# Kernel tuning notes

Measured on AMD Instinct MI355X. Metric: run time of the kernel, lower is better.

## Reference

```python
import jax, jax.numpy as jnp
import numpy as np

B, S, D = 2, 2048, 1024
H, HD = 16, 64
G, E, M = 2, 8, 1024
EPS = 1e-5


def setup_inputs() -> dict:
    key = jax.random.key(0)
    ks = jax.random.split(key, 20)
    s = 0.02
    return {
        "input": jax.random.normal(ks[0], (B, S, D), jnp.float32),
        "Wq": s * jax.random.normal(ks[1], (D, H * HD), jnp.float32),
        "bq": jnp.zeros((H * HD,), jnp.float32),
        "Wk": s * jax.random.normal(ks[2], (D, H * HD), jnp.float32),
        "bk": jnp.zeros((H * HD,), jnp.float32),
        "Wv": s * jax.random.normal(ks[3], (D, H * HD), jnp.float32),
        "bv": jnp.zeros((H * HD,), jnp.float32),
        "Wo": s * jax.random.normal(ks[4], (H * HD, D), jnp.float32),
        "bo": jnp.zeros((D,), jnp.float32),
        "ln1_g": jnp.ones((D,), jnp.float32),
        "ln1_b": jnp.zeros((D,), jnp.float32),
        "gate_W": s * jax.random.normal(ks[5], (G, D, E), jnp.float32),
        "gate_b": jnp.zeros((G, E), jnp.float32),
        "eW1": s * jax.random.normal(ks[6], (G, E, D, M), jnp.float32),
        "eb1": jnp.zeros((G, E, M), jnp.float32),
        "eW2": s * jax.random.normal(ks[7], (G, E, M, D), jnp.float32),
        "eb2": jnp.zeros((G, E, D), jnp.float32),
        "ln2_g": jnp.ones((D,), jnp.float32),
        "ln2_b": jnp.zeros((D,), jnp.float32),
    }


def _layer_norm(x, g, b):
    mu = jnp.mean(x, axis=-1, keepdims=True)
    var = jnp.mean(jnp.square(x - mu), axis=-1, keepdims=True)
    return (x - mu) * jax.lax.rsqrt(var + EPS) * g + b


def _attention(x, Wq, bq, Wk, bk, Wv, bv, Wo, bo):
    q = (x @ Wq + bq).reshape(B, S, H, HD)
    k = (x @ Wk + bk).reshape(B, S, H, HD)
    v = (x @ Wv + bv).reshape(B, S, H, HD)
    scores = jnp.einsum("bqhd,bkhd->bhqk", q, k) * (1.0 / np.sqrt(HD))
    causal = jnp.tril(jnp.ones((S, S), bool))  # block_size tril mask
    scores = jnp.where(causal, scores, jnp.float32(-1e9))
    probs = jax.nn.softmax(scores, axis=-1)
    out = jnp.einsum("bhqk,bkhd->bqhd", probs, v).reshape(B, S, H * HD)
    return out @ Wo + bo


def _moe(h, gate_W, gate_b, eW1, eb1, eW2, eb2):
    # per-gate softmax over that gate's experts
    gates = jax.nn.softmax(jnp.einsum("bsd,gde->bsge", h, gate_W) + gate_b, axis=-1)
    hid = jax.nn.relu(jnp.einsum("bsd,gedm->bsgem", h, eW1) + eb1)
    exp_out = jnp.einsum("bsgem,gemd->bsged", hid, eW2) + eb2
    # gate-weighted combine, averaged over the n_gates gates
    return jnp.einsum("bsge,bsged->bsd", gates, exp_out) / G


def reference(input, Wq, bq, Wk, bk, Wv, bv, Wo, bo, ln1_g, ln1_b,
              gate_W, gate_b, eW1, eb1, eW2, eb2, ln2_g, ln2_b):
    attn = _attention(input, Wq, bq, Wk, bk, Wv, bv, Wo, bo)
    normed = _layer_norm(attn + input, ln1_g, ln1_b)
    moe_out = _moe(normed, gate_W, gate_b, eW1, eb1, eW2, eb2)
    return _layer_norm(moe_out + normed, ln2_g, ln2_b)
```

## Files before the change

kernel.cpp:

```cpp
#include <hip/hip_runtime.h>

#define BB 2
#define SS 2048
#define DD 1024
#define HH 16
#define HDD 64
#define TT 4096
#define GG 2
#define EE 8
#define MM 1024
#define NEXP 16

typedef __bf16 bf16;
typedef __attribute__((ext_vector_type(8))) __bf16 bf16x8;
typedef __attribute__((ext_vector_type(4))) float f32x4;

__device__ __forceinline__ void async_ld16(void* lds, const void* g) {
  __builtin_amdgcn_global_load_lds((const __attribute__((address_space(1))) unsigned int*)g,
                                   (__attribute__((address_space(3))) unsigned int*)lds,
                                   16, 0, 0);
}

static const long OFF_WQKVT = 0;
static const long OFF_WOT   = OFF_WQKVT + 6291456L;
static const long OFF_W1T   = OFF_WOT   + 2097152L;
static const long OFF_W2T   = OFF_W1T   + 33554432L;
static const long OFF_XBF   = OFF_W2T   + 33554432L;
static const long OFF_REGA  = OFF_XBF   + 8388608L;
static const long OFF_H1F   = OFF_REGA  + 33554432L;
static const long OFF_H1B   = OFF_H1F   + 16777216L;
static const long OFF_GATES = OFF_H1B   + 8388608L;
static const long OFF_BQKV  = OFF_GATES + 262144L;
static const long OFF_MOE   = OFF_BQKV  + 12288L;
static const long WS_NEED   = OFF_MOE   + 16777216L;

__global__ void cast_f32_bf16(const float* __restrict__ in, bf16* __restrict__ out, long n) {
  long idx = ((long)blockIdx.x * blockDim.x + threadIdx.x) * 4;
  if (idx + 3 < n) {
    float4 v = *(const float4*)(in + idx);
    out[idx]   = (bf16)v.x; out[idx+1] = (bf16)v.y;
    out[idx+2] = (bf16)v.z; out[idx+3] = (bf16)v.w;
  }
}

__global__ void transpose_cast(const float* __restrict__ in, bf16* __restrict__ out,
                               int R, int C, long in_zstride, long out_zoff, long out_ld) {
  __shared__ float tile[32][33];
  int z = blockIdx.z;
  const float* src = in + (long)z * in_zstride;
  bf16* dst = out + (long)z * out_zoff;
  int c0 = blockIdx.x * 32, r0 = blockIdx.y * 32;
  int tx = threadIdx.x, ty = threadIdx.y;
  for (int i = 0; i < 4; i++) {
    int r = ty + i * 8;
    tile[r][tx] = src[(long)(r0 + r) * C + c0 + tx];
  }
  __syncthreads();
  for (int i = 0; i < 4; i++) {
    int n = ty + i * 8;
    dst[(long)(c0 + n) * out_ld + r0 + tx] = (bf16)tile[tx][n];
  }
}

__global__ void transpose_cast4(const float* __restrict__ s0, const float* __restrict__ s1,
                                const float* __restrict__ s2, const float* __restrict__ s3,
                                bf16* __restrict__ d0, bf16* __restrict__ d1,
                                bf16* __restrict__ d2, bf16* __restrict__ d3) {
  __shared__ float tile[32][33];
  int z = blockIdx.z;
  const float* src = (z == 0) ? s0 : (z == 1) ? s1 : (z == 2) ? s2 : s3;
  bf16* dst = (z == 0) ? d0 : (z == 1) ? d1 : (z == 2) ? d2 : d3;
  int c0 = blockIdx.x * 32, r0 = blockIdx.y * 32;
  int tx = threadIdx.x, ty = threadIdx.y;
  for (int i = 0; i < 4; i++) {
    int r = ty + i * 8;
    tile[r][tx] = src[(long)(r0 + r) * 1024 + c0 + tx];
  }
  __syncthreads();
  for (int i = 0; i < 4; i++) {
    int n = ty + i * 8;
    dst[(long)(c0 + n) * 1024 + r0 + tx] = (bf16)tile[tx][n];
  }
}

__global__ void pack3(const float* __restrict__ a, const float* __restrict__ b,
                      const float* __restrict__ c, float* __restrict__ out, int n) {
  int i = blockIdx.x * blockDim.x + threadIdx.x;
  if (i < n) out[i] = a[i];
  else if (i < 2 * n) out[i] = b[i - n];
  else if (i < 3 * n) out[i] = c[i - 2 * n];
}

template<int EPI>
__global__ __launch_bounds__(256, 3)
void gemm_bt(const bf16* __restrict__ A, const bf16* __restrict__ BT,
             int M, int N, int K, int lda, int ldb,
             const float* __restrict__ bias, int bias_off,
             const float* __restrict__ resid,
             const float* __restrict__ gates, int gate_base,
             float* __restrict__ outf, bf16* __restrict__ outb, int ldo,
             float* __restrict__ p1a, float* __restrict__ p1b) {
  __shared__ bf16 As[128 * 64];
  __shared__ bf16 Bs[128 * 64];
  int gx = gridDim.x, gy = gridDim.y;
  int l = blockIdx.x + gx * blockIdx.y;
  int xcd = l & 7, idx = l >> 3;
  int RG = gx >> 2, CG = gy >> 1;
  int bmB = (xcd >> 1) * RG + (idx % RG);
  int bnB = (xcd & 1) * CG + (idx / RG);
  int bm = bmB * 128;
  int bn = bnB * 128;
  long koff = (long)blockIdx.z * K;
  A += koff; BT += koff;
  int tid = threadIdx.x;
  int wave = tid >> 6, lane = tid & 63;
  int quad = lane >> 4, l16 = lane & 15;
  int wr = wave >> 1, wc = wave & 1;

  f32x4 acc[4][4];
  for (int i = 0; i < 4; i++)
    for (int j = 0; j < 4; j++) acc[i][j] = (f32x4){0.f, 0.f, 0.f, 0.f};

  for (int k0 = 0; k0 < K; k0 += 64) {
    __syncthreads();
    for (int i = 0; i < 4; i++) {
      int s = (i * 4 + wave) * 64 + lane;
      int r = s >> 3, cp = s & 7, c = cp ^ (r & 7);
      async_ld16((char*)As + s * 16, A + (long)(bm + r) * lda + k0 + c * 8);
      async_ld16((char*)Bs + s * 16, BT + (long)(bn + r) * ldb + k0 + c * 8);
    }
    __syncthreads();
    for (int kk = 0; kk < 64; kk += 32) {
      int cc = quad + (kk >> 3);
      bf16x8 af[4], bfr[4];
      for (int i = 0; i < 4; i++) {
        int row = wr * 64 + i * 16 + l16;
        af[i] = *(const bf16x8*)((char*)As + row * 128 + (cc ^ (row & 7)) * 16);
      }
      for (int j = 0; j < 4; j++) {
        int row = wc * 64 + j * 16 + l16;
        bfr[j] = *(const bf16x8*)((char*)Bs + row * 128 + (cc ^ (row & 7)) * 16);
      }
      for (int i = 0; i < 4; i++)
        for (int j = 0; j < 4; j++)
          acc[i][j] = __builtin_amdgcn_mfma_f32_16x16x32_bf16(af[i], bfr[j], acc[i][j], 0, 0, 0);
    }
  }

  float* dst = outf;
  if (EPI == 3 && blockIdx.z == 1)
    dst = (bm < 2048) ? p1a : (p1b - 2048L * 1024);

  for (int i = 0; i < 4; i++)
    for (int j = 0; j < 4; j++) {
      int colg = bn + wc * 64 + j * 16 + l16;
      for (int r = 0; r < 4; r++) {
        int rowg = bm + wr * 64 + i * 16 + quad * 4 + r;
        float v = acc[i][j][r];
        if (EPI == 0) {
          v += bias[colg];
          outb[(long)rowg * ldo + colg] = (bf16)v;
        } else if (EPI == 1) {
          v += bias[colg] + resid[(long)rowg * ldo + colg];
          outf[(long)rowg * ldo + colg] = v;
        } else if (EPI == 2) {
          v += bias[bias_off + colg];
          v = v > 0.f ? v : 0.f;
          float gsc = gates[(long)rowg * NEXP + gate_base + (colg >> 10)] * 0.5f;
          outb[(long)rowg * ldo + colg] = (bf16)(v * gsc);
        } else {
          dst[(long)rowg * ldo + colg] += v;
        }
      }
    }
}

#define VPAD 132
__global__ __launch_bounds__(256, 3)
void flash_attn(const bf16* __restrict__ qkv, bf16* __restrict__ attn) {
  int qbp = blockIdx.y & 15;
  int bh = blockIdx.x + 8 * (blockIdx.y >> 4);
  int b = bh >> 4, h = bh & 15;
  int tid = threadIdx.x;
  int wave = tid >> 6, lane = tid & 63, quad = lane >> 4, l16 = lane & 15;

  __shared__ bf16 Ks[128 * 64];
  __shared__ bf16 Vt[64][VPAD];
  __shared__ bf16 VsPs[4 * 16 * VPAD];
  bf16* Vs = VsPs;
  bf16* PsB = VsPs;

  const long rs = 3072;
  const bf16* Qp = qkv + (long)b * SS * rs + (long)h * HDD;
  const bf16* Kp = Qp + 1024;
  const bf16* Vp = Qp + 2048;

  for (int half = 0; half < 2; half++) {
    int qb = half ? qbp : (31 - qbp);
    bf16x8 qf[2];
    {
      int qrow = qb * 64 + wave * 16 + l16;
      for (int c = 0; c < 2; c++)
        qf[c] = *(const bf16x8*)(Qp + (long)qrow * rs + c * 32 + quad * 8);
    }
    f32x4 o[4];
    for (int j = 0; j < 4; j++) o[j] = (f32x4){0.f, 0.f, 0.f, 0.f};
    float lrow[4] = {0.f, 0.f, 0.f, 0.f};

    int niter = (qb >> 1) + 1;
    for (int kt = 0; kt < niter; kt++) {
      __syncthreads();
      for (int i = 0; i < 4; i++) {
        int s = (i * 4 + wave) * 64 + lane;
        int r = s >> 3, cp = s & 7, c = cp ^ (r & 7);
        async_ld16((char*)Ks + s * 16, Kp + (long)(kt * 128 + r) * rs + c * 8);
        async_ld16((char*)Vs + s * 16, Vp + (long)(kt * 128 + r) * rs + c * 8);
      }
      __syncthreads();

      {
        int d = lane, kb = wave * 32;
        bf16 tmp[32];
        for (int k2 = 0; k2 < 32; k2++) {
          int k = kb + k2;
          tmp[k2] = *((const bf16*)((char*)Vs + k * 128 + (((d >> 3) ^ (k & 7)) * 16) + (d & 7) * 2));
        }
        for (int j = 0; j < 4; j++)
          *(bf16x8*)(&Vt[d][kb + j * 8]) = *(bf16x8*)(&tmp[j * 8]);
      }

      f32x4 s8[8];
      for (int n = 0; n < 8; n++) s8[n] = (f32x4){0.f, 0.f, 0.f, 0.f};
      for (int c = 0; c < 2; c++) {
        int cc = quad + c * 4;
        for (int n = 0; n < 8; n++) {
          int row = n * 16 + l16;
          bf16x8 kf = *(const bf16x8*)((char*)Ks + row * 128 + (cc ^ (row & 7)) * 16);
          s8[n] = __builtin_amdgcn_mfma_f32_16x16x32_bf16(qf[c], kf, s8[n], 0, 0, 0);
        }
      }

      const float sc = 0.125f;
      const float M0 = 12.0f;
      float psum[4] = {0.f, 0.f, 0.f, 0.f};
      if (kt == niter - 1) {
        for (int n = 0; n < 8; n++) {
          int key = kt * 128 + n * 16 + l16;
          for (int r = 0; r < 4; r++) {
            int q = qb * 64 + wave * 16 + quad * 4 + r;
            float e = (key <= q) ? __expf(s8[n][r] * sc - M0) : 0.f;
            s8[n][r] = e; psum[r] += e;
          }
        }
      } else {
        for (int n = 0; n < 8; n++)
          for (int r = 0; r < 4; r++) {
            float e = __expf(s8[n][r] * sc - M0);
            s8[n][r] = e; psum[r] += e;
          }
      }
      for (int r = 0; r < 4; r++) {
        for (int d2 = 1; d2 < 16; d2 <<= 1) psum[r] += __shfl_xor(psum[r], d2, 64);
        lrow[r] += psum[r];
      }

      __syncthreads();

      for (int n = 0; n < 8; n++)
        for (int r = 0; r < 4; r++)
          PsB[(wave * 16 + quad * 4 + r) * VPAD + n * 16 + l16] = (bf16)s8[n][r];
      for (int c = 0; c < 4; c++) {
        bf16x8 pf = *(const bf16x8*)(&PsB[(wave * 16 + l16) * VPAD + c * 32 + quad * 8]);
        for (int j = 0; j < 4; j++) {
          bf16x8 vf = *(const bf16x8*)(&Vt[j * 16 + l16][c * 32 + quad * 8]);
          o[j] = __builtin_amdgcn_mfma_f32_16x16x32_bf16(pf, vf, o[j], 0, 0, 0);
        }
      }
    }

    for (int j = 0; j < 4; j++)
      for (int r = 0; r < 4; r++) {
        int t = b * SS + qb * 64 + wave * 16 + quad * 4 + r;
        int col = h * 64 + j * 16 + l16;
        attn[(long)t * 1024 + col] = (bf16)(o[j][r] / lrow[r]);
      }
  }
}

__global__ __launch_bounds__(256)
void layernorm(const float* __restrict__ in, const float* __restrict__ resid,
               const float* __restrict__ p1a, const float* __restrict__ p1b,
               const float* __restrict__ g, const float* __restrict__ b,
               float* __restrict__ outf, bf16* __restrict__ outb) {
  int row = blockIdx.x;
  int tid = threadIdx.x;
  const float* x = in + (long)row * DD;
  const float* ex = nullptr;
  if (p1a) ex = (row < 2048) ? (p1a + (long)row * DD) : (p1b + (long)(row - 2048) * DD);
  float v[4];
  for (int i = 0; i < 4; i++) {
    int c = tid + i * 256;
    v[i] = x[c];
    if (resid) v[i] += resid[(long)row * DD + c];
    if (ex) v[i] += ex[c];
  }
  __shared__ float red[8];
  float s = v[0] + v[1] + v[2] + v[3];
  for (int d = 1; d < 64; d <<= 1) s += __shfl_xor(s, d, 64);
  if ((tid & 63) == 0) red[tid >> 6] = s;
  __syncthreads();
  float mean = (red[0] + red[1] + red[2] + red[3]) * (1.0f / DD);
  float s2 = 0.f;
  for (int i = 0; i < 4; i++) { float d = v[i] - mean; s2 += d * d; }
  for (int d = 1; d < 64; d <<= 1) s2 += __shfl_xor(s2, d, 64);
  if ((tid & 63) == 0) red[4 + (tid >> 6)] = s2;
  __syncthreads();
  float var = (red[4] + red[5] + red[6] + red[7]) * (1.0f / DD);
  float rstd = rsqrtf(var + 1e-5f);
  for (int i = 0; i < 4; i++) {
    int c = tid + i * 256;
    float y = (v[i] - mean) * rstd * g[c] + b[c];
    if (outf) outf[(long)row * DD + c] = y;
    if (outb) outb[(long)row * DD + c] = (bf16)y;
  }
}

__global__ __launch_bounds__(256)
void gate_moe_init(const float* __restrict__ h, const float* __restrict__ gW,
                   const float* __restrict__ gb, const float* __restrict__ eb2,
                   float* __restrict__ gates, float* __restrict__ moe,
                   float* __restrict__ p1a, float* __restrict__ p1b) {
  int wave = threadIdx.x >> 6, lane = threadIdx.x & 63;
  int t = blockIdx.x * 4 + wave;
  float acc[16];
  for (int i = 0; i < 16; i++) acc[i] = 0.f;
  for (int kk = 0; kk < 16; kk++) {
    int k = lane + kk * 64;
    float xv = h[(long)t * DD + k];
    for (int g2 = 0; g2 < 2; g2++)
      for (int e = 0; e < 8; e++)
        acc[g2 * 8 + e] += xv * gW[(long)g2 * DD * EE + (long)k * EE + e];
  }
  for (int i = 0; i < 16; i++)
    for (int d = 1; d < 64; d <<= 1) acc[i] += __shfl_xor(acc[i], d, 64);
  __shared__ float gsh[4][16];
  if (lane == 0) {
    float out[16];
    for (int g2 = 0; g2 < 2; g2++) {
      float mx = -1e30f;
      for (int e = 0; e < 8; e++) { acc[g2 * 8 + e] += gb[g2 * 8 + e]; mx = fmaxf(mx, acc[g2 * 8 + e]); }
      float sum = 0.f;
      for (int e = 0; e < 8; e++) { out[g2 * 8 + e] = __expf(acc[g2 * 8 + e] - mx); sum += out[g2 * 8 + e]; }
      for (int e = 0; e < 8; e++) out[g2 * 8 + e] /= sum;
    }
    for (int i = 0; i < 16; i++) { gsh[wave][i] = out[i]; gates[(long)t * 16 + i] = out[i]; }
  }
  __syncthreads();
  float gr[16];
  for (int i = 0; i < 16; i++) gr[i] = gsh[wave][i];
  float* mrow = moe + (long)t * DD;
  float* prow = (t < 2048) ? (p1a + (long)t * DD) : (p1b + (long)(t - 2048) * DD);
  for (int i = 0; i < 16; i++) {
    int d = lane + i * 64;
    float s = 0.f;
    for (int ge = 0; ge < 16; ge++) s += gr[ge] * eb2[ge * 1024 + d];
    mrow[d] = s * 0.5f;
    prow[d] = 0.f;
  }
}

extern "C" void kernel_launch(void* const* d_in, const int* in_sizes, int n_in,
                              void* d_out, int out_size, void* d_ws, size_t ws_size,
                              hipStream_t stream) {
  const float* X     = (const float*)d_in[0];
  const float* Wq    = (const float*)d_in[1];
  const float* bq    = (const float*)d_in[2];
  const float* Wk    = (const float*)d_in[3];
  const float* bk    = (const float*)d_in[4];
  const float* Wv    = (const float*)d_in[5];
  const float* bv    = (const float*)d_in[6];
  const float* Wo    = (const float*)d_in[7];
  const float* bo    = (const float*)d_in[8];
  const float* ln1g  = (const float*)d_in[9];
  const float* ln1b  = (const float*)d_in[10];
  const float* gateW = (const float*)d_in[11];
  const float* gateb = (const float*)d_in[12];
  const float* eW1   = (const float*)d_in[13];
  const float* eb1   = (const float*)d_in[14];
  const float* eW2   = (const float*)d_in[15];
  const float* eb2   = (const float*)d_in[16];
  const float* ln2g  = (const float*)d_in[17];
  const float* ln2b  = (const float*)d_in[18];

  if (ws_size < (size_t)WS_NEED) return;

  char* ws = (char*)d_ws;
  bf16* WqkvT  = (bf16*)(ws + OFF_WQKVT);
  bf16* WoT    = (bf16*)(ws + OFF_WOT);
  bf16* W1T    = (bf16*)(ws + OFF_W1T);
  bf16* W2T    = (bf16*)(ws + OFF_W2T);
  bf16* Xbf    = (bf16*)(ws + OFF_XBF);
  bf16* qkvb   = (bf16*)(ws + OFF_REGA);
  bf16* attnb  = (bf16*)(ws + OFF_REGA + 25165824L);
  bf16* hid    = (bf16*)(ws + OFF_REGA);
  float* h1f   = (float*)(ws + OFF_H1F);
  bf16* h1b    = (bf16*)(ws + OFF_H1B);
  float* gates = (float*)(ws + OFF_GATES);
  float* bqkv  = (float*)(ws + OFF_BQKV);
  float* moe   = (float*)(ws + OFF_MOE);
  float* p1a   = (float*)(ws + OFF_WQKVT);
  float* p1b   = (float*)(ws + OFF_XBF);

  dim3 tcb(32, 8);
  transpose_cast4<<<dim3(32, 32, 4), tcb, 0, stream>>>(Wq, Wk, Wv, Wo,
                                                       WqkvT, WqkvT + 1024L * 1024,
                                                       WqkvT + 2048L * 1024, WoT);
  transpose_cast<<<dim3(32, 32, 16), tcb, 0, stream>>>(eW1, W1T, 1024, 1024, 1048576L, 1048576L, 1024);
  transpose_cast<<<dim3(32, 32, 16), tcb, 0, stream>>>(eW2, W2T, 1024, 1024, 1048576L, 1024L, 16384);
  cast_f32_bf16<<<4096, 256, 0, stream>>>(X, Xbf, 4194304L);
  pack3<<<12, 256, 0, stream>>>(bq, bk, bv, bqkv, 1024);

  gemm_bt<0><<<dim3(32, 24, 1), 256, 0, stream>>>(Xbf, WqkvT, TT, 3072, 1024, 1024, 1024,
                                                  bqkv, 0, nullptr, nullptr, 0, nullptr, qkvb, 3072, nullptr, nullptr);
  flash_attn<<<dim3(8, 64), 256, 0, stream>>>(qkvb, attnb);
  gemm_bt<1><<<dim3(32, 8, 1), 256, 0, stream>>>(attnb, WoT, TT, 1024, 1024, 1024, 1024,
                                                 bo, 0, X, nullptr, 0, moe, nullptr, 1024, nullptr, nullptr);
  layernorm<<<4096, 256, 0, stream>>>(moe, nullptr, nullptr, nullptr, ln1g, ln1b, h1f, h1b);
  gate_moe_init<<<1024, 256, 0, stream>>>(h1f, gateW, gateb, eb2, gates, moe, p1a, p1b);
  for (int c = 0; c < 4; c++) {
    gemm_bt<2><<<dim3(32, 32, 1), 256, 0, stream>>>(h1b, W1T + (long)c * 4096 * 1024, TT, 4096, 1024, 1024, 1024,
                                                    eb1, c * 4096, nullptr, gates, c * 4, nullptr, hid, 4096, nullptr, nullptr);
    gemm_bt<3><<<dim3(32, 8, 2), 256, 0, stream>>>(hid, W2T + (long)c * 4096, TT, 1024, 2048, 4096, 16384,
                                                   nullptr, 0, nullptr, nullptr, 0, moe, nullptr, 1024, p1a, p1b);
  }
  layernorm<<<4096, 256, 0, stream>>>(moe, h1f, p1a, p1b, ln2g, ln2b, (float*)d_out, nullptr);
}
```

Baseline: 778.8 us.

## Pre-transpose V globally, split-K Wo GEMM, fold expert bias into final layernorm

A new vtrans kernel writes V transposed to global memory, so flash attention can async-load V^T tiles straight into LDS. This removes the per-tile in-LDS V transpose and one barrier, and P is now staged through a per-wave transposed buffer. The Wo projection becomes a split-K GEMM whose second partial is summed inside layernorm1. The eb2 gate-weighted bias and the moe/partial zero-init move out of the gate kernel: the first W2 chunk stores instead of accumulating, and the bias is added in the final layernorm. The two expert transpose launches are merged into one. This adds an extra kernel and global traffic for V^T, and LDS reads for the P fragment are now scalar gathers.

New measurement: 807.2 us. 1.04x slower.

```diff
diff --git a/kernel.cpp b/kernel.cpp
--- a/kernel.cpp
+++ b/kernel.cpp
@@ -13,6 +13,7 @@
 
 typedef __bf16 bf16;
 typedef __attribute__((ext_vector_type(8))) __bf16 bf16x8;
+typedef __attribute__((ext_vector_type(4))) __bf16 bf16x4;
 typedef __attribute__((ext_vector_type(4))) float f32x4;
 
 __device__ __forceinline__ void async_ld16(void* lds, const void* g) {
@@ -43,25 +44,6 @@
   }
 }
 
-__global__ void transpose_cast(const float* __restrict__ in, bf16* __restrict__ out,
-                               int R, int C, long in_zstride, long out_zoff, long out_ld) {
-  __shared__ float tile[32][33];
-  int z = blockIdx.z;
-  const float* src = in + (long)z * in_zstride;
-  bf16* dst = out + (long)z * out_zoff;
-  int c0 = blockIdx.x * 32, r0 = blockIdx.y * 32;
-  int tx = threadIdx.x, ty = threadIdx.y;
-  for (int i = 0; i < 4; i++) {
-    int r = ty + i * 8;
-    tile[r][tx] = src[(long)(r0 + r) * C + c0 + tx];
-  }
-  __syncthreads();
-  for (int i = 0; i < 4; i++) {
-    int n = ty + i * 8;
-    dst[(long)(c0 + n) * out_ld + r0 + tx] = (bf16)tile[tx][n];
-  }
-}
-
 __global__ void transpose_cast4(const float* __restrict__ s0, const float* __restrict__ s1,
                                 const float* __restrict__ s2, const float* __restrict__ s3,
                                 bf16* __restrict__ d0, bf16* __restrict__ d1,
@@ -83,12 +65,51 @@
   }
 }
 
+__global__ void transpose_experts(const float* __restrict__ eW1, const float* __restrict__ eW2,
+                                  bf16* __restrict__ W1T, bf16* __restrict__ W2T) {
+  __shared__ float tile[32][33];
+  int z = blockIdx.z;
+  const float* src; bf16* dstp; long ld;
+  if (z < 16) { src = eW1 + (long)z * 1048576; dstp = W1T + (long)z * 1048576; ld = 1024; }
+  else        { src = eW2 + (long)(z - 16) * 1048576; dstp = W2T + (long)(z - 16) * 1024; ld = 16384; }
+  int c0 = blockIdx.x * 32, r0 = blockIdx.y * 32;
+  int tx = threadIdx.x, ty = threadIdx.y;
+  for (int i = 0; i < 4; i++) {
+    int r = ty + i * 8;
+    tile[r][tx] = src[(long)(r0 + r) * 1024 + c0 + tx];
+  }
+  __syncthreads();
+  for (int i = 0; i < 4; i++) {
+    int n = ty + i * 8;
+    dstp[(long)(c0 + n) * ld + r0 + tx] = (bf16)tile[tx][n];
+  }
+}
+
 __global__ void pack3(const float* __restrict__ a, const float* __restrict__ b,
                       const float* __restrict__ c, float* __restrict__ out, int n) {
   int i = blockIdx.x * blockDim.x + threadIdx.x;
   if (i < n) out[i] = a[i];
   else if (i < 2 * n) out[i] = b[i - n];
   else if (i < 3 * n) out[i] = c[i - 2 * n];
+}
+
+__global__ void vtrans(const bf16* __restrict__ qkv, bf16* __restrict__ vtg) {
+  __shared__ bf16 T[128][72];
+  int bh = blockIdx.x, s0 = blockIdx.y * 128;
+  int b = bh >> 4, h = bh & 15;
+  const bf16* Vp = qkv + (long)b * SS * 3072 + 2048 + h * 64;
+  int tid = threadIdx.x;
+  for (int i = 0; i < 4; i++) {
+    int idx = tid + i * 256; int r = idx >> 3, c = idx & 7;
+    *(bf16x8*)&T[r][c * 8] = *(const bf16x8*)(Vp + (long)(s0 + r) * 3072 + c * 8);
+  }
+  __syncthreads();
+  for (int i = 0; i < 4; i++) {
+    int idx = tid + i * 256; int d = idx >> 4, sc = idx & 15;
+    bf16 tmp[8];
+    for (int j = 0; j < 8; j++) tmp[j] = T[sc * 8 + j][d];
+    *(bf16x8*)(vtg + ((long)bh * 64 + d) * 2048 + s0 + sc * 8) = *(bf16x8*)tmp;
+  }
 }
 
 template<int EPI>
@@ -106,10 +127,8 @@
   int l = blockIdx.x + gx * blockIdx.y;
   int xcd = l & 7, idx = l >> 3;
   int RG = gx >> 2, CG = gy >> 1;
-  int bmB = (xcd >> 1) * RG + (idx % RG);
-  int bnB = (xcd & 1) * CG + (idx / RG);
-  int bm = bmB * 128;
-  int bn = bnB * 128;
+  int bm = ((xcd >> 1) * RG + (idx % RG)) * 128;
+  int bn = ((xcd & 1) * CG + (idx / RG)) * 128;
   long koff = (long)blockIdx.z * K;
   A += koff; BT += koff;
   int tid = threadIdx.x;
@@ -148,7 +167,7 @@
   }
 
   float* dst = outf;
-  if (EPI == 3 && blockIdx.z == 1)
+  if ((EPI == 3 || EPI == 4) && blockIdx.z == 1)
     dst = (bm < 2048) ? p1a : (p1b - 2048L * 1024);
 
   for (int i = 0; i < 4; i++)
@@ -161,23 +180,29 @@
           v += bias[colg];
           outb[(long)rowg * ldo + colg] = (bf16)v;
         } else if (EPI == 1) {
-          v += bias[colg] + resid[(long)rowg * ldo + colg];
-          outf[(long)rowg * ldo + colg] = v;
+          if (blockIdx.z == 0) {
+            v += bias[colg] + resid[(long)rowg * ldo + colg];
+            outf[(long)rowg * ldo + colg] = v;
+          } else {
+            p1a[(long)rowg * ldo + colg] = v;
+          }
         } else if (EPI == 2) {
           v += bias[bias_off + colg];
           v = v > 0.f ? v : 0.f;
           float gsc = gates[(long)rowg * NEXP + gate_base + (colg >> 10)] * 0.5f;
           outb[(long)rowg * ldo + colg] = (bf16)(v * gsc);
+        } else if (EPI == 3) {
+          dst[(long)rowg * ldo + colg] += v;
         } else {
-          dst[(long)rowg * ldo + colg] += v;
+          dst[(long)rowg * ldo + colg] = v;
         }
       }
     }
 }
 
-#define VPAD 132
 __global__ __launch_bounds__(256, 3)
-void flash_attn(const bf16* __restrict__ qkv, bf16* __restrict__ attn) {
+void flash_attn(const bf16* __restrict__ qkv, const bf16* __restrict__ vtg,
+                bf16* __restrict__ attn) {
   int qbp = blockIdx.y & 15;
   int bh = blockIdx.x + 8 * (blockIdx.y >> 4);
   int b = bh >> 4, h = bh & 15;
@@ -185,15 +210,13 @@
   int wave = tid >> 6, lane = tid & 63, quad = lane >> 4, l16 = lane & 15;
 
   __shared__ bf16 Ks[128 * 64];
-  __shared__ bf16 Vt[64][VPAD];
-  __shared__ bf16 VsPs[4 * 16 * VPAD];
-  bf16* Vs = VsPs;
-  bf16* PsB = VsPs;
+  __shared__ bf16 VtL[64 * 128];
+  __shared__ bf16 PsT[4][128][20];
 
   const long rs = 3072;
   const bf16* Qp = qkv + (long)b * SS * rs + (long)h * HDD;
   const bf16* Kp = Qp + 1024;
-  const bf16* Vp = Qp + 2048;
+  const bf16* Vg = vtg + (long)bh * 64 * 2048;
 
   for (int half = 0; half < 2; half++) {
     int qb = half ? qbp : (31 - qbp);
@@ -214,20 +237,13 @@
         int s = (i * 4 + wave) * 64 + lane;
         int r = s >> 3, cp = s & 7, c = cp ^ (r & 7);
         async_ld16((char*)Ks + s * 16, Kp + (long)(kt * 128 + r) * rs + c * 8);
-        async_ld16((char*)Vs + s * 16, Vp + (long)(kt * 128 + r) * rs + c * 8);
+      }
+      for (int i = 0; i < 4; i++) {
+        int s = (i * 4 + wave) * 64 + lane;
+        int r = s >> 4, cp = s & 15, gc = (cp & 8) | ((cp ^ r) & 7);
+        async_ld16((char*)VtL + s * 16, Vg + (long)r * 2048 + kt * 128 + gc * 8);
       }
       __syncthreads();
-
-      {
-        int d = lane, kb = wave * 32;
-        bf16 tmp[32];
-        for (int k2 = 0; k2 < 32; k2++) {
-          int k = kb + k2;
-          tmp[k2] = *((const bf16*)((char*)Vs + k * 128 + (((d >> 3) ^ (k & 7)) * 16) + (d & 7) * 2));
-        }
-        for (int j = 0; j < 4; j++)
-          *(bf16x8*)(&Vt[d][kb + j * 8]) = *(bf16x8*)(&tmp[j * 8]);
-      }
 
       f32x4 s8[8];
       for (int n = 0; n < 8; n++) s8[n] = (f32x4){0.f, 0.f, 0.f, 0.f};
@@ -264,16 +280,20 @@
         lrow[r] += psum[r];
       }
 
-      __syncthreads();
-
-      for (int n = 0; n < 8; n++)
-        for (int r = 0; r < 4; r++)
-          PsB[(wave * 16 + quad * 4 + r) * VPAD + n * 16 + l16] = (bf16)s8[n][r];
+      for (int n = 0; n < 8; n++) {
+        bf16x4 p4;
+        for (int r = 0; r < 4; r++) p4[r] = (bf16)s8[n][r];
+        *(bf16x4*)(&PsT[wave][n * 16 + l16][quad * 4]) = p4;
+      }
       for (int c = 0; c < 4; c++) {
-        bf16x8 pf = *(const bf16x8*)(&PsB[(wave * 16 + l16) * VPAD + c * 32 + quad * 8]);
-        for (int j = 0; j < 4; j++) {
-          bf16x8 vf = *(const bf16x8*)(&Vt[j * 16 + l16][c * 32 + quad * 8]);
-          o[j] = __builtin_amdgcn_mfma_f32_16x16x32_bf16(pf, vf, o[j], 0, 0, 0);
+        bf16x8 pf;
+        for (int j = 0; j < 8; j++)
+          pf[j] = PsT[wave][c * 32 + quad * 8 + j][l16];
+        for (int j2 = 0; j2 < 4; j2++) {
+          int d = j2 * 16 + l16;
+          int k4 = c * 4 + quad;
+          bf16x8 vf = *(const bf16x8*)((char*)VtL + d * 256 + (((k4 & 8) | ((k4 ^ d) & 7)) * 16));
+          o[j2] = __builtin_amdgcn_mfma_f32_16x16x32_bf16(pf, vf, o[j2], 0, 0, 0);
         }
       }
     }
@@ -287,9 +307,11 @@
   }
 }
 
+template<bool GB>
 __global__ __launch_bounds__(256)
 void layernorm(const float* __restrict__ in, const float* __restrict__ resid,
                const float* __restrict__ p1a, const float* __restrict__ p1b,
+               const float* __restrict__ gates, const float* __restrict__ eb2,
                const float* __restrict__ g, const float* __restrict__ b,
                float* __restrict__ outf, bf16* __restrict__ outb) {
   int row = blockIdx.x;
@@ -297,12 +319,22 @@
   const float* x = in + (long)row * DD;
   const float* ex = nullptr;
   if (p1a) ex = (row < 2048) ? (p1a + (long)row * DD) : (p1b + (long)(row - 2048) * DD);
+  __shared__ float gsh[16];
+  if (GB) {
+    if (tid < 16) gsh[tid] = gates[(long)row * 16 + tid] * 0.5f;
+    __syncthreads();
+  }
   float v[4];
   for (int i = 0; i < 4; i++) {
     int c = tid + i * 256;
     v[i] = x[c];
     if (resid) v[i] += resid[(long)row * DD + c];
     if (ex) v[i] += ex[c];
+    if (GB) {
+      float s = 0.f;
+      for (int ge = 0; ge < 16; ge++) s += gsh[ge] * eb2[ge * 1024 + c];
+      v[i] += s;
+    }
   }
   __shared__ float red[8];
   float s = v[0] + v[1] + v[2] + v[3];
@@ -326,10 +358,8 @@
 }
 
 __global__ __launch_bounds__(256)
-void gate_moe_init(const float* __restrict__ h, const float* __restrict__ gW,
-                   const float* __restrict__ gb, const float* __restrict__ eb2,
-                   float* __restrict__ gates, float* __restrict__ moe,
-                   float* __restrict__ p1a, float* __restrict__ p1b) {
+void gate_kernel(const float* __restrict__ h, const float* __restrict__ gW,
+                 const float* __restrict__ gb, float* __restrict__ gates) {
   int wave = threadIdx.x >> 6, lane = threadIdx.x & 63;
   int t = blockIdx.x * 4 + wave;
   float acc[16];
@@ -343,7 +373,6 @@
   }
   for (int i = 0; i < 16; i++)
     for (int d = 1; d < 64; d <<= 1) acc[i] += __shfl_xor(acc[i], d, 64);
-  __shared__ float gsh[4][16];
   if (lane == 0) {
     float out[16];
     for (int g2 = 0; g2 < 2; g2++) {
@@ -353,19 +382,7 @@
       for (int e = 0; e < 8; e++) { out[g2 * 8 + e] = __expf(acc[g2 * 8 + e] - mx); sum += out[g2 * 8 + e]; }
       for (int e = 0; e < 8; e++) out[g2 * 8 + e] /= sum;
     }
-    for (int i = 0; i < 16; i++) { gsh[wave][i] = out[i]; gates[(long)t * 16 + i] = out[i]; }
-  }
-  __syncthreads();
-  float gr[16];
-  for (int i = 0; i < 16; i++) gr[i] = gsh[wave][i];
-  float* mrow = moe + (long)t * DD;
-  float* prow = (t < 2048) ? (p1a + (long)t * DD) : (p1b + (long)(t - 2048) * DD);
-  for (int i = 0; i < 16; i++) {
-    int d = lane + i * 64;
-    float s = 0.f;
-    for (int ge = 0; ge < 16; ge++) s += gr[ge] * eb2[ge * 1024 + d];
-    mrow[d] = s * 0.5f;
-    prow[d] = 0.f;
+    for (int i = 0; i < 16; i++) gates[(long)t * 16 + i] = out[i];
   }
 }
 
@@ -403,11 +420,13 @@
   bf16* qkvb   = (bf16*)(ws + OFF_REGA);
   bf16* attnb  = (bf16*)(ws + OFF_REGA + 25165824L);
   bf16* hid    = (bf16*)(ws + OFF_REGA);
+  float* pWo   = (float*)(ws + OFF_REGA);
   float* h1f   = (float*)(ws + OFF_H1F);
   bf16* h1b    = (bf16*)(ws + OFF_H1B);
   float* gates = (float*)(ws + OFF_GATES);
   float* bqkv  = (float*)(ws + OFF_BQKV);
   float* moe   = (float*)(ws + OFF_MOE);
+  bf16* VtG    = (bf16*)(ws + OFF_MOE);
   float* p1a   = (float*)(ws + OFF_WQKVT);
   float* p1b   = (float*)(ws + OFF_XBF);
 
@@ -415,23 +434,29 @@
   transpose_cast4<<<dim3(32, 32, 4), tcb, 0, stream>>>(Wq, Wk, Wv, Wo,
                                                        WqkvT, WqkvT + 1024L * 1024,
                                                        WqkvT + 2048L * 1024, WoT);
-  transpose_cast<<<dim3(32, 32, 16), tcb, 0, stream>>>(eW1, W1T, 1024, 1024, 1048576L, 1048576L, 1024);
-  transpose_cast<<<dim3(32, 32, 16), tcb, 0, stream>>>(eW2, W2T, 1024, 1024, 1048576L, 1024L, 16384);
+  transpose_experts<<<dim3(32, 32, 32), tcb, 0, stream>>>(eW1, eW2, W1T, W2T);
   cast_f32_bf16<<<4096, 256, 0, stream>>>(X, Xbf, 4194304L);
   pack3<<<12, 256, 0, stream>>>(bq, bk, bv, bqkv, 1024);
 
   gemm_bt<0><<<dim3(32, 24, 1), 256, 0, stream>>>(Xbf, WqkvT, TT, 3072, 1024, 1024, 1024,
                                                   bqkv, 0, nullptr, nullptr, 0, nullptr, qkvb, 3072, nullptr, nullptr);
-  flash_attn<<<dim3(8, 64), 256, 0, stream>>>(qkvb, attnb);
-  gemm_bt<1><<<dim3(32, 8, 1), 256, 0, stream>>>(attnb, WoT, TT, 1024, 1024, 1024, 1024,
-                                                 bo, 0, X, nullptr, 0, moe, nullptr, 1024, nullptr, nullptr);
-  layernorm<<<4096, 256, 0, stream>>>(moe, nullptr, nullptr, nullptr, ln1g, ln1b, h1f, h1b);
-  gate_moe_init<<<1024, 256, 0, stream>>>(h1f, gateW, gateb, eb2, gates, moe, p1a, p1b);
+  vtrans<<<dim3(32, 16), 256, 0, stream>>>(qkvb, VtG);
+  flash_attn<<<dim3(8, 64), 256, 0, stream>>>(qkvb, VtG, attnb);
+  gemm_bt<1><<<dim3(32, 8, 2), 256, 0, stream>>>(attnb, WoT, TT, 1024, 512, 1024, 1024,
+                                                 bo, 0, X, nullptr, 0, moe, nullptr, 1024, pWo, nullptr);
+  layernorm<false><<<4096, 256, 0, stream>>>(moe, nullptr, pWo, pWo + 2048L * 1024,
+                                             nullptr, nullptr, ln1g, ln1b, h1f, h1b);
+  gate_kernel<<<1024, 256, 0, stream>>>(h1f, gateW, gateb, gates);
   for (int c = 0; c < 4; c++) {
     gemm_bt<2><<<dim3(32, 32, 1), 256, 0, stream>>>(h1b, W1T + (long)c * 4096 * 1024, TT, 4096, 1024, 1024, 1024,
                                                     eb1, c * 4096, nullptr, gates, c * 4, nullptr, hid, 4096, nullptr, nullptr);
-    gemm_bt<3><<<dim3(32, 8, 2), 256, 0, stream>>>(hid, W2T + (long)c * 4096, TT, 1024, 2048, 4096, 16384,
-                                                   nullptr, 0, nullptr, nullptr, 0, moe, nullptr, 1024, p1a, p1b);
-  }
-  layernorm<<<4096, 256, 0, stream>>>(moe, h1f, p1a, p1b, ln2g, ln2b, (float*)d_out, nullptr);
-}
+    if (c == 0)
+      gemm_bt<4><<<dim3(32, 8, 2), 256, 0, stream>>>(hid, W2T + (long)c * 4096, TT, 1024, 2048, 4096, 16384,
+                                                     nullptr, 0, nullptr, nullptr, 0, moe, nullptr, 1024, p1a, p1b);
+    else
+      gemm_bt<3><<<dim3(32, 8, 2), 256, 0, stream>>>(hid, W2T + (long)c * 4096, TT, 1024, 2048, 4096, 16384,
+                                                     nullptr, 0, nullptr, nullptr, 0, moe, nullptr, 1024, p1a, p1b);
+  }
+  layernorm<true><<<4096, 256, 0, stream>>>(moe, h1f, p1a, p1b, gates, eb2,
+                                            ln2g, ln2b, (float*)d_out, nullptr);
+}
```
